# Performance work log

Hardware: AMD Instinct MI355X
Metric: run time of the kernel (lower is better)

The kernel has to match this reference:

```python
import jax, jax.numpy as jnp
import numpy as np

N_NODES = 50000
N_EDGES = 800000
D = 64
H = 128


def setup_inputs() -> dict:
    key = jax.random.key(0)
    ks = jax.random.split(key, 8)
    s = 0.05
    return {
        "nodes": jax.random.normal(ks[0], (N_NODES, D), jnp.float32),
        "edges": jax.random.normal(ks[1], (N_EDGES, D), jnp.float32),
        "We1": jax.random.normal(ks[2], (3 * D, H), jnp.float32) * s,
        "be1": jnp.zeros((H,), jnp.float32),
        "We2": jax.random.normal(ks[3], (H, D), jnp.float32) * s,
        "be2": jnp.zeros((D,), jnp.float32),
        "Wn1": jax.random.normal(ks[4], (2 * D, H), jnp.float32) * s,
        "bn1": jnp.zeros((H,), jnp.float32),
        "Wn2": jax.random.normal(ks[5], (H, D), jnp.float32) * s,
        "bn2": jnp.zeros((D,), jnp.float32),
        "senders": jax.random.randint(ks[6], (N_EDGES,), 0, N_NODES, jnp.int32),
        "receivers": jax.random.randint(ks[7], (N_EDGES,), 0, N_NODES, jnp.int32),
    }


def reference(nodes, edges, We1, be1, We2, be2, Wn1, bn1, Wn2, bn2, senders, receivers):
    # EdgeBlock(use_globals=False): concat[edge, receiver_node, sender_node] -> MLP
    edge_in = jnp.concatenate([edges, nodes[receivers], nodes[senders]], axis=-1)  # [E, 3D]
    h = jax.nn.relu(edge_in @ We1 + be1)
    new_edges = h @ We2 + be2  # [E, D]

    # NodeBlock(use_sent_edges=False, use_globals=False):
    # aggregate received edges via segment_sum, concat with node feats -> MLP
    agg = jax.ops.segment_sum(new_edges, receivers, num_segments=nodes.shape[0])  # [N, D]
    node_in = jnp.concatenate([agg, nodes], axis=-1)  # [N, 2D]
    h2 = jax.nn.relu(node_in @ Wn1 + bn1)
    new_nodes = h2 @ Wn2 + bn2  # [N, D]
    return new_nodes
```

## Files before the change

### kernel.cpp

```cpp
#include <hip/hip_runtime.h>

#define NN 50000
#define NE 800000

typedef __attribute__((ext_vector_type(8))) short bf16x8;
typedef __attribute__((ext_vector_type(8))) unsigned short us8;
typedef __attribute__((ext_vector_type(4))) unsigned short us4;
typedef __attribute__((ext_vector_type(4))) float f32x4;

#define MFMA16 __builtin_amdgcn_mfma_f32_16x16x32_bf16

__device__ __forceinline__ unsigned short f2b(float f) {
    union { float f; unsigned int u; } x; x.f = f;
    unsigned int r = x.u + 0x7FFFu + ((x.u >> 16) & 1u);
    return (unsigned short)(r >> 16);
}

__global__ __launch_bounds__(256) void prep_kernel(
    const float* __restrict__ nodes,
    const float* __restrict__ We1, const float* __restrict__ We2,
    const float* __restrict__ Wn1, const float* __restrict__ Wn2,
    unsigned short* __restrict__ nodes_bf,
    unsigned short* __restrict__ We1T, unsigned short* __restrict__ We2T,
    unsigned short* __restrict__ Wn1T, unsigned short* __restrict__ Wn2T)
{
    const int b = blockIdx.x, t = threadIdx.x;
    if (b < 400) {
        const float4* src = (const float4*)nodes;
        for (int i = b * 256 + t; i < NN * 16; i += 400 * 256) {
            float4 v = src[i];
            us4 o; o[0] = f2b(v.x); o[1] = f2b(v.y); o[2] = f2b(v.z); o[3] = f2b(v.w);
            *(us4*)&nodes_bf[(size_t)i * 4] = o;
        }
    } else {
        const int base = (b - 400) * 256 + t;
        for (int idx = base; idx < 57344; idx += 16 * 256) {
            if (idx < 24576) {
                int n = idx / 192, k = idx % 192;
                We1T[idx] = f2b(We1[k * 128 + n]);
            } else if (idx < 32768) {
                int j = idx - 24576; int n = j / 128, k = j % 128;
                We2T[j] = f2b(We2[k * 64 + n]);
            } else if (idx < 49152) {
                int j = idx - 32768; int n = j / 128, k = j % 128;
                Wn1T[j] = f2b(Wn1[k * 128 + n]);
            } else {
                int j = idx - 49152; int n = j / 128, k = j % 128;
                Wn2T[j] = f2b(Wn2[k * 64 + n]);
            }
        }
    }
}

__global__ __launch_bounds__(256, 4) void edge_kernel(
    const unsigned short* __restrict__ nodes_bf, const float* __restrict__ edges,
    const unsigned short* __restrict__ We1T, const float* __restrict__ be1,
    const unsigned short* __restrict__ We2T, const float* __restrict__ be2,
    const int* __restrict__ senders, const int* __restrict__ receivers,
    float* __restrict__ agg)
{
    __shared__ unsigned short xs[64 * 200];
    __shared__ unsigned short wb[128 * 40];
    __shared__ int ridx[64];
    __shared__ int sidx[64];

    const int t = threadIdx.x;
    const int e0 = blockIdx.x * 64;
    const int w = t >> 6;
    const int l = t & 63;
    const int lc = l & 15;
    const int lq = l >> 4;

    if (t < 64) { ridx[t] = receivers[e0 + t]; sidx[t] = senders[e0 + t]; }
    __syncthreads();

    #pragma unroll
    for (int i = 0; i < 4; ++i) {
        int idx = t + 256 * i;
        int m = idx >> 4, q = idx & 15;
        float4 v = *(const float4*)&edges[((size_t)(e0 + m)) * 64 + q * 4];
        us4 o; o[0] = f2b(v.x); o[1] = f2b(v.y); o[2] = f2b(v.z); o[3] = f2b(v.w);
        *(us4*)&xs[m * 200 + q * 4] = o;
    }
    #pragma unroll
    for (int i = 0; i < 2; ++i) {
        int idx = t + 256 * i;
        int m = idx >> 3, q = idx & 7;
        us8 v = *(const us8*)&nodes_bf[(size_t)ridx[m] * 64 + q * 8];
        *(us8*)&xs[m * 200 + 64 + q * 8] = v;
    }
    #pragma unroll
    for (int i = 0; i < 2; ++i) {
        int idx = t + 256 * i;
        int m = idx >> 3, q = idx & 7;
        us8 v = *(const us8*)&nodes_bf[(size_t)sidx[m] * 64 + q * 8];
        *(us8*)&xs[m * 200 + 128 + q * 8] = v;
    }
    __syncthreads();

    f32x4 acc[4][2];
    #pragma unroll
    for (int mt = 0; mt < 4; ++mt) { acc[mt][0] = (f32x4)0.f; acc[mt][1] = (f32x4)0.f; }

    for (int c = 0; c < 6; ++c) {
        const int k0 = 32 * c;
        #pragma unroll
        for (int i = 0; i < 2; ++i) {
            int idx = t + 256 * i;
            int n = idx >> 2, cc = idx & 3;
            *(us8*)&wb[n * 40 + cc * 8] = *(const us8*)&We1T[n * 192 + k0 + cc * 8];
        }
        __syncthreads();
        bf16x8 b0 = *(const bf16x8*)&wb[(w * 32 + lc) * 40 + lq * 8];
        bf16x8 b1 = *(const bf16x8*)&wb[(w * 32 + 16 + lc) * 40 + lq * 8];
        #pragma unroll
        for (int mt = 0; mt < 4; ++mt) {
            bf16x8 a = *(const bf16x8*)&xs[(mt * 16 + lc) * 200 + k0 + lq * 8];
            acc[mt][0] = MFMA16(a, b0, acc[mt][0], 0, 0, 0);
            acc[mt][1] = MFMA16(a, b1, acc[mt][1], 0, 0, 0);
        }
        __syncthreads();
    }

    #pragma unroll
    for (int nt = 0; nt < 2; ++nt) {
        int col = w * 32 + nt * 16 + lc;
        float bias = be1[col];
        #pragma unroll
        for (int mt = 0; mt < 4; ++mt) {
            #pragma unroll
            for (int r = 0; r < 4; ++r) {
                int row = mt * 16 + lq * 4 + r;
                float v = fmaxf(acc[mt][nt][r] + bias, 0.f);
                xs[row * 136 + col] = f2b(v);
            }
        }
    }
    __syncthreads();

    f32x4 acc2[4];
    #pragma unroll
    for (int mt = 0; mt < 4; ++mt) acc2[mt] = (f32x4)0.f;

    for (int c = 0; c < 4; ++c) {
        const int k0 = 32 * c;
        {
            int n = t >> 2, cc = t & 3;
            *(us8*)&wb[n * 40 + cc * 8] = *(const us8*)&We2T[n * 128 + k0 + cc * 8];
        }
        __syncthreads();
        bf16x8 b = *(const bf16x8*)&wb[(w * 16 + lc) * 40 + lq * 8];
        #pragma unroll
        for (int mt = 0; mt < 4; ++mt) {
            bf16x8 a = *(const bf16x8*)&xs[(mt * 16 + lc) * 136 + k0 + lq * 8];
            acc2[mt] = MFMA16(a, b, acc2[mt], 0, 0, 0);
        }
        __syncthreads();
    }

    const int col = w * 16 + lc;
    const float bias2 = be2[col];
    #pragma unroll
    for (int mt = 0; mt < 4; ++mt) {
        #pragma unroll
        for (int r = 0; r < 4; ++r) {
            int row = mt * 16 + lq * 4 + r;
            atomicAdd(&agg[(size_t)ridx[row] * 64 + col], acc2[mt][r] + bias2);
        }
    }
}

__global__ __launch_bounds__(256, 4) void node_kernel(
    const unsigned short* __restrict__ nodes_bf, const float* __restrict__ agg,
    const unsigned short* __restrict__ Wn1T, const float* __restrict__ bn1,
    const unsigned short* __restrict__ Wn2T, const float* __restrict__ bn2,
    float* __restrict__ out)
{
    __shared__ unsigned short xs[64 * 136];
    __shared__ unsigned short wb[128 * 40];

    const int t = threadIdx.x;
    const int n0 = blockIdx.x * 64;
    const int w = t >> 6;
    const int l = t & 63;
    const int lc = l & 15;
    const int lq = l >> 4;

    #pragma unroll
    for (int i = 0; i < 4; ++i) {
        int idx = t + 256 * i;
        int m = idx >> 4, q = idx & 15;
        int n = n0 + m;
        float4 v = make_float4(0.f, 0.f, 0.f, 0.f);
        if (n < NN) v = *(const float4*)&agg[(size_t)n * 64 + q * 4];
        us4 o; o[0] = f2b(v.x); o[1] = f2b(v.y); o[2] = f2b(v.z); o[3] = f2b(v.w);
        *(us4*)&xs[m * 136 + q * 4] = o;
    }
    #pragma unroll
    for (int i = 0; i < 2; ++i) {
        int idx = t + 256 * i;
        int m = idx >> 3, q = idx & 7;
        int n = n0 + m;
        us8 v = {0, 0, 0, 0, 0, 0, 0, 0};
        if (n < NN) v = *(const us8*)&nodes_bf[(size_t)n * 64 + q * 8];
        *(us8*)&xs[m * 136 + 64 + q * 8] = v;
    }
    __syncthreads();

    f32x4 acc[4][2];
    #pragma unroll
    for (int mt = 0; mt < 4; ++mt) { acc[mt][0] = (f32x4)0.f; acc[mt][1] = (f32x4)0.f; }

    for (int c = 0; c < 4; ++c) {
        const int k0 = 32 * c;
        #pragma unroll
        for (int i = 0; i < 2; ++i) {
            int idx = t + 256 * i;
            int n = idx >> 2, cc = idx & 3;
            *(us8*)&wb[n * 40 + cc * 8] = *(const us8*)&Wn1T[n * 128 + k0 + cc * 8];
        }
        __syncthreads();
        bf16x8 b0 = *(const bf16x8*)&wb[(w * 32 + lc) * 40 + lq * 8];
        bf16x8 b1 = *(const bf16x8*)&wb[(w * 32 + 16 + lc) * 40 + lq * 8];
        #pragma unroll
        for (int mt = 0; mt < 4; ++mt) {
            bf16x8 a = *(const bf16x8*)&xs[(mt * 16 + lc) * 136 + k0 + lq * 8];
            acc[mt][0] = MFMA16(a, b0, acc[mt][0], 0, 0, 0);
            acc[mt][1] = MFMA16(a, b1, acc[mt][1], 0, 0, 0);
        }
        __syncthreads();
    }

    #pragma unroll
    for (int nt = 0; nt < 2; ++nt) {
        int col = w * 32 + nt * 16 + lc;
        float bias = bn1[col];
        #pragma unroll
        for (int mt = 0; mt < 4; ++mt) {
            #pragma unroll
            for (int r = 0; r < 4; ++r) {
                int row = mt * 16 + lq * 4 + r;
                float v = fmaxf(acc[mt][nt][r] + bias, 0.f);
                xs[row * 136 + col] = f2b(v);
            }
        }
    }
    __syncthreads();

    f32x4 acc2[4];
    #pragma unroll
    for (int mt = 0; mt < 4; ++mt) acc2[mt] = (f32x4)0.f;

    for (int c = 0; c < 4; ++c) {
        const int k0 = 32 * c;
        {
            int n = t >> 2, cc = t & 3;
            *(us8*)&wb[n * 40 + cc * 8] = *(const us8*)&Wn2T[n * 128 + k0 + cc * 8];
        }
        __syncthreads();
        bf16x8 b = *(const bf16x8*)&wb[(w * 16 + lc) * 40 + lq * 8];
        #pragma unroll
        for (int mt = 0; mt < 4; ++mt) {
            bf16x8 a = *(const bf16x8*)&xs[(mt * 16 + lc) * 136 + k0 + lq * 8];
            acc2[mt] = MFMA16(a, b, acc2[mt], 0, 0, 0);
        }
        __syncthreads();
    }

    const int col = w * 16 + lc;
    const float bias2 = bn2[col];
    #pragma unroll
    for (int mt = 0; mt < 4; ++mt) {
        #pragma unroll
        for (int r = 0; r < 4; ++r) {
            int row = mt * 16 + lq * 4 + r;
            int n = n0 + row;
            if (n < NN) out[(size_t)n * 64 + col] = acc2[mt][r] + bias2;
        }
    }
}

extern "C" void kernel_launch(void* const* d_in, const int* in_sizes, int n_in,
                              void* d_out, int out_size, void* d_ws, size_t ws_size,
                              hipStream_t stream) {
    const float* nodes = (const float*)d_in[0];
    const float* edges = (const float*)d_in[1];
    const float* We1   = (const float*)d_in[2];
    const float* be1   = (const float*)d_in[3];
    const float* We2   = (const float*)d_in[4];
    const float* be2   = (const float*)d_in[5];
    const float* Wn1   = (const float*)d_in[6];
    const float* bn1   = (const float*)d_in[7];
    const float* Wn2   = (const float*)d_in[8];
    const float* bn2   = (const float*)d_in[9];
    const int* senders   = (const int*)d_in[10];
    const int* receivers = (const int*)d_in[11];
    float* out = (float*)d_out;

    char* ws = (char*)d_ws;
    float* agg = (float*)ws;
    unsigned short* nodes_bf = (unsigned short*)(ws + 12800000);
    unsigned short* We1T = (unsigned short*)(ws + 19200000);
    unsigned short* We2T = (unsigned short*)(ws + 19249152);
    unsigned short* Wn1T = (unsigned short*)(ws + 19265536);
    unsigned short* Wn2T = (unsigned short*)(ws + 19298304);

    hipMemsetAsync(agg, 0, (size_t)NN * 64 * sizeof(float), stream);
    prep_kernel<<<416, 256, 0, stream>>>(nodes, We1, We2, Wn1, Wn2,
                                         nodes_bf, We1T, We2T, Wn1T, Wn2T);
    edge_kernel<<<NE / 64, 256, 0, stream>>>(nodes_bf, edges, We1T, be1, We2T, be2,
                                             senders, receivers, agg);
    node_kernel<<<(NN + 63) / 64, 256, 0, stream>>>(nodes_bf, agg, Wn1T, bn1, Wn2T, bn2, out);
}
```

Before: 463.0 us.

## Use register-resident weights, direct-gather MFMA and packed bf16 atomics for aggregation

The edge and node kernels now keep the first-layer weight fragments in registers and feed gathered edge and node rows straight into MFMA, with no LDS staging and fewer barriers. The edge kernel becomes persistent, with 3125 blocks each looping over 4 tiles. The second GEMM is transposed so each wave writes a contiguous row. The segment-sum accumulator changes from fp32 to bf16 with packed v2bf16 atomic adds, which halves atomic traffic and the memset but loses accumulation precision across about 16 edges per node.

```diff
diff --git a/kernel.cpp b/kernel.cpp
--- a/kernel.cpp
+++ b/kernel.cpp
@@ -2,11 +2,13 @@
 
 #define NN 50000
 #define NE 800000
+#define NTILE_E 12500
 
 typedef __attribute__((ext_vector_type(8))) short bf16x8;
 typedef __attribute__((ext_vector_type(8))) unsigned short us8;
 typedef __attribute__((ext_vector_type(4))) unsigned short us4;
 typedef __attribute__((ext_vector_type(4))) float f32x4;
+typedef __attribute__((ext_vector_type(2))) short s16x2;
 
 #define MFMA16 __builtin_amdgcn_mfma_f32_16x16x32_bf16
 
@@ -14,6 +16,12 @@
     union { float f; unsigned int u; } x; x.f = f;
     unsigned int r = x.u + 0x7FFFu + ((x.u >> 16) & 1u);
     return (unsigned short)(r >> 16);
+}
+
+__device__ __forceinline__ void atomic_pk_bf16(unsigned short* addr, float a, float b) {
+    s16x2 v; v[0] = (short)f2b(a); v[1] = (short)f2b(b);
+    __builtin_amdgcn_global_atomic_fadd_v2bf16(
+        (__attribute__((address_space(1))) s16x2*)(unsigned long long)addr, v);
 }
 
 __global__ __launch_bounds__(256) void prep_kernel(
@@ -57,225 +65,201 @@
     const unsigned short* __restrict__ We1T, const float* __restrict__ be1,
     const unsigned short* __restrict__ We2T, const float* __restrict__ be2,
     const int* __restrict__ senders, const int* __restrict__ receivers,
-    float* __restrict__ agg)
+    unsigned short* __restrict__ agg)
 {
-    __shared__ unsigned short xs[64 * 200];
-    __shared__ unsigned short wb[128 * 40];
-    __shared__ int ridx[64];
-    __shared__ int sidx[64];
+    __shared__ unsigned short hs[64 * 136];
+    __shared__ unsigned short w2[64 * 136];
 
     const int t = threadIdx.x;
-    const int e0 = blockIdx.x * 64;
-    const int w = t >> 6;
-    const int l = t & 63;
-    const int lc = l & 15;
-    const int lq = l >> 4;
-
-    if (t < 64) { ridx[t] = receivers[e0 + t]; sidx[t] = senders[e0 + t]; }
-    __syncthreads();
+    const int w = t >> 6, l = t & 63, lc = l & 15, lq = l >> 4;
 
     #pragma unroll
     for (int i = 0; i < 4; ++i) {
         int idx = t + 256 * i;
-        int m = idx >> 4, q = idx & 15;
-        float4 v = *(const float4*)&edges[((size_t)(e0 + m)) * 64 + q * 4];
-        us4 o; o[0] = f2b(v.x); o[1] = f2b(v.y); o[2] = f2b(v.z); o[3] = f2b(v.w);
-        *(us4*)&xs[m * 200 + q * 4] = o;
-    }
-    #pragma unroll
-    for (int i = 0; i < 2; ++i) {
-        int idx = t + 256 * i;
-        int m = idx >> 3, q = idx & 7;
-        us8 v = *(const us8*)&nodes_bf[(size_t)ridx[m] * 64 + q * 8];
-        *(us8*)&xs[m * 200 + 64 + q * 8] = v;
-    }
-    #pragma unroll
-    for (int i = 0; i < 2; ++i) {
-        int idx = t + 256 * i;
-        int m = idx >> 3, q = idx & 7;
-        us8 v = *(const us8*)&nodes_bf[(size_t)sidx[m] * 64 + q * 8];
-        *(us8*)&xs[m * 200 + 128 + q * 8] = v;
-    }
+        int n = idx >> 4, q = idx & 15;
+        *(us8*)&w2[n * 136 + q * 8] = *(const us8*)&We2T[n * 128 + q * 8];
+    }
+
+    bf16x8 b1[6][2];
+    #pragma unroll
+    for (int c = 0; c < 6; ++c)
+        #pragma unroll
+        for (int j = 0; j < 2; ++j)
+            b1[c][j] = *(const bf16x8*)&We1T[(size_t)(w * 32 + j * 16 + lc) * 192 + c * 32 + lq * 8];
+    const float be1a = be1[w * 32 + lc];
+    const float be1b = be1[w * 32 + 16 + lc];
+
     __syncthreads();
 
-    f32x4 acc[4][2];
-    #pragma unroll
-    for (int mt = 0; mt < 4; ++mt) { acc[mt][0] = (f32x4)0.f; acc[mt][1] = (f32x4)0.f; }
-
-    for (int c = 0; c < 6; ++c) {
-        const int k0 = 32 * c;
-        #pragma unroll
-        for (int i = 0; i < 2; ++i) {
-            int idx = t + 256 * i;
-            int n = idx >> 2, cc = idx & 3;
-            *(us8*)&wb[n * 40 + cc * 8] = *(const us8*)&We1T[n * 192 + k0 + cc * 8];
-        }
+    for (int tile = blockIdx.x; tile < NTILE_E; tile += gridDim.x) {
+        const int e0 = tile * 64;
+        int rn[4], sn[4];
+        #pragma unroll
+        for (int mt = 0; mt < 4; ++mt) {
+            rn[mt] = receivers[e0 + mt * 16 + lc];
+            sn[mt] = senders[e0 + mt * 16 + lc];
+        }
+
+        f32x4 acc0[4], acc1v[4];
+        #pragma unroll
+        for (int mt = 0; mt < 4; ++mt) { acc0[mt] = (f32x4)0.f; acc1v[mt] = (f32x4)0.f; }
+
+        #pragma unroll
+        for (int mt = 0; mt < 4; ++mt) {
+            const float* ep = &edges[(size_t)(e0 + mt * 16 + lc) * 64 + lq * 8];
+            #pragma unroll
+            for (int c = 0; c < 2; ++c) {
+                float4 p0 = *(const float4*)(ep + c * 32);
+                float4 p1 = *(const float4*)(ep + c * 32 + 4);
+                us8 u; u[0] = f2b(p0.x); u[1] = f2b(p0.y); u[2] = f2b(p0.z); u[3] = f2b(p0.w);
+                       u[4] = f2b(p1.x); u[5] = f2b(p1.y); u[6] = f2b(p1.z); u[7] = f2b(p1.w);
+                bf16x8 af = (bf16x8)u;
+                acc0[mt]  = MFMA16(af, b1[c][0], acc0[mt], 0, 0, 0);
+                acc1v[mt] = MFMA16(af, b1[c][1], acc1v[mt], 0, 0, 0);
+            }
+            const unsigned short* rp = &nodes_bf[(size_t)rn[mt] * 64 + lq * 8];
+            #pragma unroll
+            for (int c = 0; c < 2; ++c) {
+                bf16x8 af = *(const bf16x8*)(rp + c * 32);
+                acc0[mt]  = MFMA16(af, b1[2 + c][0], acc0[mt], 0, 0, 0);
+                acc1v[mt] = MFMA16(af, b1[2 + c][1], acc1v[mt], 0, 0, 0);
+            }
+            const unsigned short* sp = &nodes_bf[(size_t)sn[mt] * 64 + lq * 8];
+            #pragma unroll
+            for (int c = 0; c < 2; ++c) {
+                bf16x8 af = *(const bf16x8*)(sp + c * 32);
+                acc0[mt]  = MFMA16(af, b1[4 + c][0], acc0[mt], 0, 0, 0);
+                acc1v[mt] = MFMA16(af, b1[4 + c][1], acc1v[mt], 0, 0, 0);
+            }
+        }
+
         __syncthreads();
-        bf16x8 b0 = *(const bf16x8*)&wb[(w * 32 + lc) * 40 + lq * 8];
-        bf16x8 b1 = *(const bf16x8*)&wb[(w * 32 + 16 + lc) * 40 + lq * 8];
-        #pragma unroll
-        for (int mt = 0; mt < 4; ++mt) {
-            bf16x8 a = *(const bf16x8*)&xs[(mt * 16 + lc) * 200 + k0 + lq * 8];
-            acc[mt][0] = MFMA16(a, b0, acc[mt][0], 0, 0, 0);
-            acc[mt][1] = MFMA16(a, b1, acc[mt][1], 0, 0, 0);
-        }
-        __syncthreads();
-    }
-
-    #pragma unroll
-    for (int nt = 0; nt < 2; ++nt) {
-        int col = w * 32 + nt * 16 + lc;
-        float bias = be1[col];
-        #pragma unroll
-        for (int mt = 0; mt < 4; ++mt) {
+        #pragma unroll
+        for (int mt = 0; mt < 4; ++mt)
             #pragma unroll
             for (int r = 0; r < 4; ++r) {
                 int row = mt * 16 + lq * 4 + r;
-                float v = fmaxf(acc[mt][nt][r] + bias, 0.f);
-                xs[row * 136 + col] = f2b(v);
-            }
-        }
-    }
-    __syncthreads();
-
-    f32x4 acc2[4];
-    #pragma unroll
-    for (int mt = 0; mt < 4; ++mt) acc2[mt] = (f32x4)0.f;
-
-    for (int c = 0; c < 4; ++c) {
-        const int k0 = 32 * c;
-        {
-            int n = t >> 2, cc = t & 3;
-            *(us8*)&wb[n * 40 + cc * 8] = *(const us8*)&We2T[n * 128 + k0 + cc * 8];
-        }
+                hs[row * 136 + w * 32 + lc]      = f2b(fmaxf(acc0[mt][r] + be1a, 0.f));
+                hs[row * 136 + w * 32 + 16 + lc] = f2b(fmaxf(acc1v[mt][r] + be1b, 0.f));
+            }
         __syncthreads();
-        bf16x8 b = *(const bf16x8*)&wb[(w * 16 + lc) * 40 + lq * 8];
-        #pragma unroll
-        for (int mt = 0; mt < 4; ++mt) {
-            bf16x8 a = *(const bf16x8*)&xs[(mt * 16 + lc) * 136 + k0 + lq * 8];
-            acc2[mt] = MFMA16(a, b, acc2[mt], 0, 0, 0);
-        }
-        __syncthreads();
-    }
-
-    const int col = w * 16 + lc;
-    const float bias2 = be2[col];
-    #pragma unroll
-    for (int mt = 0; mt < 4; ++mt) {
-        #pragma unroll
-        for (int r = 0; r < 4; ++r) {
-            int row = mt * 16 + lq * 4 + r;
-            atomicAdd(&agg[(size_t)ridx[row] * 64 + col], acc2[mt][r] + bias2);
+
+        f32x4 acc2[4];
+        #pragma unroll
+        for (int nt = 0; nt < 4; ++nt) acc2[nt] = (f32x4)0.f;
+        #pragma unroll
+        for (int c = 0; c < 4; ++c) {
+            bf16x8 bf = *(const bf16x8*)&hs[(w * 16 + lc) * 136 + c * 32 + lq * 8];
+            #pragma unroll
+            for (int nt = 0; nt < 4; ++nt) {
+                bf16x8 af = *(const bf16x8*)&w2[(nt * 16 + lc) * 136 + c * 32 + lq * 8];
+                acc2[nt] = MFMA16(af, bf, acc2[nt], 0, 0, 0);
+            }
+        }
+
+        const int node = rn[w];
+        unsigned short* ap = &agg[(size_t)node * 64];
+        #pragma unroll
+        for (int nt = 0; nt < 4; ++nt) {
+            int col = nt * 16 + lq * 4;
+            float4 bias = *(const float4*)&be2[col];
+            atomic_pk_bf16(ap + col,     acc2[nt][0] + bias.x, acc2[nt][1] + bias.y);
+            atomic_pk_bf16(ap + col + 2, acc2[nt][2] + bias.z, acc2[nt][3] + bias.w);
         }
     }
 }
 
 __global__ __launch_bounds__(256, 4) void node_kernel(
-    const unsigned short* __restrict__ nodes_bf, const float* __restrict__ agg,
+    const unsigned short* __restrict__ nodes_bf, const unsigned short* __restrict__ agg,
     const unsigned short* __restrict__ Wn1T, const float* __restrict__ bn1,
     const unsigned short* __restrict__ Wn2T, const float* __restrict__ bn2,
     float* __restrict__ out)
 {
-    __shared__ unsigned short xs[64 * 136];
-    __shared__ unsigned short wb[128 * 40];
+    __shared__ unsigned short hs[64 * 136];
+    __shared__ unsigned short w2[64 * 136];
 
     const int t = threadIdx.x;
+    const int w = t >> 6, l = t & 63, lc = l & 15, lq = l >> 4;
     const int n0 = blockIdx.x * 64;
-    const int w = t >> 6;
-    const int l = t & 63;
-    const int lc = l & 15;
-    const int lq = l >> 4;
 
     #pragma unroll
     for (int i = 0; i < 4; ++i) {
         int idx = t + 256 * i;
-        int m = idx >> 4, q = idx & 15;
-        int n = n0 + m;
-        float4 v = make_float4(0.f, 0.f, 0.f, 0.f);
-        if (n < NN) v = *(const float4*)&agg[(size_t)n * 64 + q * 4];
-        us4 o; o[0] = f2b(v.x); o[1] = f2b(v.y); o[2] = f2b(v.z); o[3] = f2b(v.w);
-        *(us4*)&xs[m * 136 + q * 4] = o;
-    }
-    #pragma unroll
-    for (int i = 0; i < 2; ++i) {
-        int idx = t + 256 * i;
-        int m = idx >> 3, q = idx & 7;
-        int n = n0 + m;
-        us8 v = {0, 0, 0, 0, 0, 0, 0, 0};
-        if (n < NN) v = *(const us8*)&nodes_bf[(size_t)n * 64 + q * 8];
-        *(us8*)&xs[m * 136 + 64 + q * 8] = v;
-    }
+        int n = idx >> 4, q = idx & 15;
+        *(us8*)&w2[n * 136 + q * 8] = *(const us8*)&Wn2T[n * 128 + q * 8];
+    }
+
+    bf16x8 b1[4][2];
+    #pragma unroll
+    for (int c = 0; c < 4; ++c)
+        #pragma unroll
+        for (int j = 0; j < 2; ++j)
+            b1[c][j] = *(const bf16x8*)&Wn1T[(size_t)(w * 32 + j * 16 + lc) * 128 + c * 32 + lq * 8];
+    const float bn1a = bn1[w * 32 + lc];
+    const float bn1b = bn1[w * 32 + 16 + lc];
+
     __syncthreads();
 
-    f32x4 acc[4][2];
-    #pragma unroll
-    for (int mt = 0; mt < 4; ++mt) { acc[mt][0] = (f32x4)0.f; acc[mt][1] = (f32x4)0.f; }
-
-    for (int c = 0; c < 4; ++c) {
-        const int k0 = 32 * c;
-        #pragma unroll
-        for (int i = 0; i < 2; ++i) {
-            int idx = t + 256 * i;
-            int n = idx >> 2, cc = idx & 3;
-            *(us8*)&wb[n * 40 + cc * 8] = *(const us8*)&Wn1T[n * 128 + k0 + cc * 8];
-        }
-        __syncthreads();
-        bf16x8 b0 = *(const bf16x8*)&wb[(w * 32 + lc) * 40 + lq * 8];
-        bf16x8 b1 = *(const bf16x8*)&wb[(w * 32 + 16 + lc) * 40 + lq * 8];
-        #pragma unroll
-        for (int mt = 0; mt < 4; ++mt) {
-            bf16x8 a = *(const bf16x8*)&xs[(mt * 16 + lc) * 136 + k0 + lq * 8];
-            acc[mt][0] = MFMA16(a, b0, acc[mt][0], 0, 0, 0);
-            acc[mt][1] = MFMA16(a, b1, acc[mt][1], 0, 0, 0);
-        }
-        __syncthreads();
-    }
-
-    #pragma unroll
-    for (int nt = 0; nt < 2; ++nt) {
-        int col = w * 32 + nt * 16 + lc;
-        float bias = bn1[col];
-        #pragma unroll
-        for (int mt = 0; mt < 4; ++mt) {
-            #pragma unroll
-            for (int r = 0; r < 4; ++r) {
-                int row = mt * 16 + lq * 4 + r;
-                float v = fmaxf(acc[mt][nt][r] + bias, 0.f);
-                xs[row * 136 + col] = f2b(v);
-            }
-        }
-    }
-    __syncthreads();
-
-    f32x4 acc2[4];
-    #pragma unroll
-    for (int mt = 0; mt < 4; ++mt) acc2[mt] = (f32x4)0.f;
-
-    for (int c = 0; c < 4; ++c) {
-        const int k0 = 32 * c;
-        {
-            int n = t >> 2, cc = t & 3;
-            *(us8*)&wb[n * 40 + cc * 8] = *(const us8*)&Wn2T[n * 128 + k0 + cc * 8];
-        }
-        __syncthreads();
-        bf16x8 b = *(const bf16x8*)&wb[(w * 16 + lc) * 40 + lq * 8];
-        #pragma unroll
-        for (int mt = 0; mt < 4; ++mt) {
-            bf16x8 a = *(const bf16x8*)&xs[(mt * 16 + lc) * 136 + k0 + lq * 8];
-            acc2[mt] = MFMA16(a, b, acc2[mt], 0, 0, 0);
-        }
-        __syncthreads();
-    }
-
-    const int col = w * 16 + lc;
-    const float bias2 = bn2[col];
+    f32x4 acc0[4], acc1v[4];
+    #pragma unroll
+    for (int mt = 0; mt < 4; ++mt) { acc0[mt] = (f32x4)0.f; acc1v[mt] = (f32x4)0.f; }
+
     #pragma unroll
     for (int mt = 0; mt < 4; ++mt) {
+        int row = n0 + mt * 16 + lc;
+        bool ok = row < NN;
+        const unsigned short* apz = &agg[(size_t)row * 64 + lq * 8];
+        const unsigned short* npz = &nodes_bf[(size_t)row * 64 + lq * 8];
+        #pragma unroll
+        for (int c = 0; c < 2; ++c) {
+            us8 z = {0,0,0,0,0,0,0,0};
+            bf16x8 af = ok ? *(const bf16x8*)(apz + c * 32) : (bf16x8)z;
+            acc0[mt]  = MFMA16(af, b1[c][0], acc0[mt], 0, 0, 0);
+            acc1v[mt] = MFMA16(af, b1[c][1], acc1v[mt], 0, 0, 0);
+        }
+        #pragma unroll
+        for (int c = 0; c < 2; ++c) {
+            us8 z = {0,0,0,0,0,0,0,0};
+            bf16x8 af = ok ? *(const bf16x8*)(npz + c * 32) : (bf16x8)z;
+            acc0[mt]  = MFMA16(af, b1[2 + c][0], acc0[mt], 0, 0, 0);
+            acc1v[mt] = MFMA16(af, b1[2 + c][1], acc1v[mt], 0, 0, 0);
+        }
+    }
+
+    #pragma unroll
+    for (int mt = 0; mt < 4; ++mt)
         #pragma unroll
         for (int r = 0; r < 4; ++r) {
             int row = mt * 16 + lq * 4 + r;
-            int n = n0 + row;
-            if (n < NN) out[(size_t)n * 64 + col] = acc2[mt][r] + bias2;
+            hs[row * 136 + w * 32 + lc]      = f2b(fmaxf(acc0[mt][r] + bn1a, 0.f));
+            hs[row * 136 + w * 32 + 16 + lc] = f2b(fmaxf(acc1v[mt][r] + bn1b, 0.f));
+        }
+    __syncthreads();
+
+    f32x4 acc2[4];
+    #pragma unroll
+    for (int nt = 0; nt < 4; ++nt) acc2[nt] = (f32x4)0.f;
+    #pragma unroll
+    for (int c = 0; c < 4; ++c) {
+        bf16x8 bf = *(const bf16x8*)&hs[(w * 16 + lc) * 136 + c * 32 + lq * 8];
+        #pragma unroll
+        for (int nt = 0; nt < 4; ++nt) {
+            bf16x8 af = *(const bf16x8*)&w2[(nt * 16 + lc) * 136 + c * 32 + lq * 8];
+            acc2[nt] = MFMA16(af, bf, acc2[nt], 0, 0, 0);
+        }
+    }
+
+    const int row = n0 + w * 16 + lc;
+    if (row < NN) {
+        float* op = &out[(size_t)row * 64];
+        #pragma unroll
+        for (int nt = 0; nt < 4; ++nt) {
+            int col = nt * 16 + lq * 4;
+            float4 bias = *(const float4*)&bn2[col];
+            float4 v;
+            v.x = acc2[nt][0] + bias.x; v.y = acc2[nt][1] + bias.y;
+            v.z = acc2[nt][2] + bias.z; v.w = acc2[nt][3] + bias.w;
+            *(float4*)(op + col) = v;
         }
     }
 }
@@ -298,17 +282,17 @@
     float* out = (float*)d_out;
 
     char* ws = (char*)d_ws;
-    float* agg = (float*)ws;
-    unsigned short* nodes_bf = (unsigned short*)(ws + 12800000);
-    unsigned short* We1T = (unsigned short*)(ws + 19200000);
-    unsigned short* We2T = (unsigned short*)(ws + 19249152);
-    unsigned short* Wn1T = (unsigned short*)(ws + 19265536);
-    unsigned short* Wn2T = (unsigned short*)(ws + 19298304);
-
-    hipMemsetAsync(agg, 0, (size_t)NN * 64 * sizeof(float), stream);
+    unsigned short* agg      = (unsigned short*)ws;
+    unsigned short* nodes_bf = (unsigned short*)(ws + 6400000);
+    unsigned short* We1T = (unsigned short*)(ws + 12800000);
+    unsigned short* We2T = (unsigned short*)(ws + 12849152);
+    unsigned short* Wn1T = (unsigned short*)(ws + 12865536);
+    unsigned short* Wn2T = (unsigned short*)(ws + 12898304);
+
+    hipMemsetAsync(agg, 0, (size_t)NN * 64 * sizeof(unsigned short), stream);
     prep_kernel<<<416, 256, 0, stream>>>(nodes, We1, We2, Wn1, Wn2,
                                          nodes_bf, We1T, We2T, Wn1T, Wn2T);
-    edge_kernel<<<NE / 64, 256, 0, stream>>>(nodes_bf, edges, We1T, be1, We2T, be2,
-                                             senders, receivers, agg);
-    node_kernel<<<(NN + 63) / 64, 256, 0, stream>>>(nodes_bf, agg, Wn1T, bn1, Wn2T, bn2, out);
-}
+    edge_kernel<<<3125, 256, 0, stream>>>(nodes_bf, edges, We1T, be1, We2T, be2,
+                                          senders, receivers, agg);
+    node_kernel<<<782, 256, 0, stream>>>(nodes_bf, agg, Wn1T, bn1, Wn2T, bn2, out);
+}
```

New measurement: 691.3 us. 49.3% more time.
